# Kernel tuning notes

Hardware: AMD Instinct MI355X
Metric: run time of the kernel (lower is better)

Reference implementation:

```python
import jax, jax.numpy as jnp
import numpy as np

WS = 8        # window_size
OWIN = 12     # overlap_win_size = int(8*0.5)+8
PAD = 2       # (OWIN - WS)//2
HEADS = 4
DH = 16
INNER = HEADS * DH  # 64
DIM = 64


def _unfold(x, ws=WS, owin=OWIN, pad=PAD):
    # torch nn.Unfold(kernel=(owin,owin), stride=ws, padding=pad):
    # output [b, C*owin*owin, L] with channel ordering (c, kh, kw), L row-major over windows
    b, c, h, w = x.shape
    xp = jnp.pad(x, ((0, 0), (0, 0), (pad, pad), (pad, pad)))
    nH, nW = h // ws, w // ws
    ri = (jnp.arange(nH) * ws)[:, None] + jnp.arange(owin)[None, :]  # [nH, owin]
    ci = (jnp.arange(nW) * ws)[:, None] + jnp.arange(owin)[None, :]  # [nW, owin]
    p = xp[:, :, ri, :]          # [b, c, nH, owin, Wp]
    p = p[:, :, :, :, ci]        # [b, c, nH, owin, nW, owin]
    p = p.transpose(0, 1, 3, 5, 2, 4)  # [b, c, kh, kw, nH, nW]
    return p.reshape(b, c * owin * owin, nH * nW)


def setup_inputs() -> dict:
    key = jax.random.key(0)
    k1, k2, k3 = jax.random.split(key, 3)
    x = jax.random.normal(k1, (1, DIM, 64, 64), jnp.float32)
    w_qkv = jax.random.normal(k2, (3 * INNER, DIM), jnp.float32) * 0.05  # 1x1 conv, no bias
    w_out = jax.random.normal(k3, (DIM, INNER), jnp.float32) * 0.05     # 1x1 conv, no bias
    ln_w = jnp.ones((DIM,), jnp.float32)
    return {"x": x, "w_qkv": w_qkv, "w_out": w_out, "ln_w": ln_w}


def reference(x, w_qkv, w_out, ln_w):
    b, c, h, w = x.shape
    # BiasFree LayerNorm over channel dim (no mean subtraction)
    xc = x.transpose(0, 2, 3, 1)                       # b h w c
    var = jnp.var(xc, axis=-1, keepdims=True)
    xn = (xc / jnp.sqrt(var + 1e-5) * ln_w).transpose(0, 3, 1, 2)
    # qkv 1x1 conv
    qkv = jnp.einsum('bchw,oc->bohw', xn, w_qkv)
    qs, ks, vs = jnp.split(qkv, 3, axis=1)
    # queries: all h*w positions
    qs = qs.transpose(0, 2, 3, 1).reshape(b, h * w, HEADS, DH).transpose(0, 2, 1, 3)  # b heads N dh
    # keys/values: overlapping unfolded windows (faithful to torch reshape order)
    kk = _unfold(ks).reshape(b, INNER, -1).reshape(b, HEADS, -1, DH)  # b heads M dh
    vv = _unfold(vs).reshape(b, INNER, -1).reshape(b, HEADS, -1, DH)
    # rel_pos and fixed_mask are all-zero tensors in the source -> no-op bias
    attn = jnp.einsum('bhnd,bhmd->bhnm', qs, kk) * (DH ** -0.5)
    attn = jax.nn.softmax(attn, axis=-1)
    out = jnp.einsum('bhnm,bhmd->bhnd', attn, vv)
    out = out.transpose(0, 2, 1, 3).reshape(b, h, w, INNER).transpose(0, 3, 1, 2)
    return jnp.einsum('bchw,oc->bohw', out, w_out)
```

## Files before the change

kernel.cpp:

```cpp
#include <hip/hip_runtime.h>
#include <math.h>

#define PIX 4096
typedef unsigned short ushort_t;
typedef unsigned int uint_t;
typedef __attribute__((ext_vector_type(8))) short bf16x8;
typedef __attribute__((ext_vector_type(16))) float f32x16;

#define OFF_USHORT 2228224
#define U_QH 0
#define U_QKB 262144
#define U_KF 786432
#define U_VF 1376256

#define QSCALE 0.36067376022224087f

#if defined(__has_builtin)
#if __has_builtin(__builtin_amdgcn_exp2f)
#define EXP2F(x) __builtin_amdgcn_exp2f(x)
#endif
#if __has_builtin(__builtin_amdgcn_perm)
#define PKHI16(u1, u0) __builtin_amdgcn_perm((u1), (u0), 0x07060302u)
#endif
#endif
#ifndef EXP2F
#define EXP2F(x) exp2f(x)
#endif
#ifndef PKHI16
#define PKHI16(u1, u0) (((u0) >> 16) | ((u1) & 0xFFFF0000u))
#endif

__device__ __forceinline__ ushort_t rn_bf16(float x) {
    uint_t u = __float_as_uint(x);
    return (ushort_t)((u + 0x7FFFu + ((u >> 16) & 1u)) >> 16);
}

__global__ __launch_bounds__(256)
void k_qkv(const float* __restrict__ x, const float* __restrict__ w_qkv,
           const float* __restrict__ ln_w, ushort_t* __restrict__ QH,
           ushort_t* __restrict__ QKB)
{
    const int tid = threadIdx.x;
    const int w = tid >> 6, l = tid & 63;
    const int col = l & 31, half = l >> 5;
    const int id = (int)blockIdx.x * 4 + w;
    const int ot = id >> 7;
    const int pt = id & 127;
    const int obase = ot * 32;
    const int gpx = pt * 32 + col;

    float s = 0.f, s2 = 0.f;
    #pragma unroll 16
    for (int c = 0; c < 64; ++c) {
        float v = x[c * PIX + gpx];
        s += v; s2 = fmaf(v, v, s2);
    }
    const float mean = s * 0.015625f;
    const float var  = fmaf(-mean, mean, s2 * 0.015625f);
    const float rs   = 1.0f / sqrtf(var + 1e-5f);

    f32x16 acc = {0,0,0,0,0,0,0,0,0,0,0,0,0,0,0,0};
    const float* wrow = w_qkv + (obase + col) * 64;
    #pragma unroll
    for (int s4 = 0; s4 < 4; ++s4) {
        const int kbase = s4 * 16 + half * 8;
        float t8[8];
        *(float4*)&t8[0] = *(const float4*)&wrow[kbase];
        *(float4*)&t8[4] = *(const float4*)&wrow[kbase + 4];
        union { uint_t u[4]; bf16x8 b; } wa;
        #pragma unroll
        for (int j = 0; j < 4; ++j)
            wa.u[j] = (uint_t)rn_bf16(t8[2 * j]) | ((uint_t)rn_bf16(t8[2 * j + 1]) << 16);
        const float4 lwa = *(const float4*)&ln_w[kbase];
        const float4 lwb = *(const float4*)&ln_w[kbase + 4];
        float b8[8];
        b8[0] = x[(kbase + 0) * PIX + gpx] * rs * lwa.x;
        b8[1] = x[(kbase + 1) * PIX + gpx] * rs * lwa.y;
        b8[2] = x[(kbase + 2) * PIX + gpx] * rs * lwa.z;
        b8[3] = x[(kbase + 3) * PIX + gpx] * rs * lwa.w;
        b8[4] = x[(kbase + 4) * PIX + gpx] * rs * lwb.x;
        b8[5] = x[(kbase + 5) * PIX + gpx] * rs * lwb.y;
        b8[6] = x[(kbase + 6) * PIX + gpx] * rs * lwb.z;
        b8[7] = x[(kbase + 7) * PIX + gpx] * rs * lwb.w;
        union { uint_t u[4]; bf16x8 b; } xb;
        #pragma unroll
        for (int j = 0; j < 4; ++j)
            xb.u[j] = (uint_t)rn_bf16(b8[2 * j]) | ((uint_t)rn_bf16(b8[2 * j + 1]) << 16);
        acc = __builtin_amdgcn_mfma_f32_32x32x16_bf16(wa.b, xb.b, acc, 0, 0, 0);
    }

    #pragma unroll
    for (int j = 0; j < 16; ++j) {
        const int o = obase + (j & 3) + 8 * (j >> 2) + 4 * half;
        if (o < 64) {
            QH[((o >> 4) * PIX + gpx) * 16 + (o & 15)] = rn_bf16(acc[j] * QSCALE);
        } else {
            QKB[(o - 64) * PIX + gpx] = rn_bf16(acc[j]);
        }
    }
}

__global__ __launch_bounds__(256)
void k_prep_kv(const ushort_t* __restrict__ QKB,
               ushort_t* __restrict__ KF, ushort_t* __restrict__ VF)
{
    const int bid = blockIdx.x;
    const int tid = threadIdx.x;
    if (bid < 288) {
        const int t = bid * 256 + tid;
        const int h = t / 18432; int r = t - h * 18432;
        const int i = r >> 6;   const int l = r & 63;
        const int col = l & 31, rl = l >> 5;
        const int m = i * 32 + col;
        const int cc = m / 576;  const int r3 = m - cc * 576;
        const int orr = r3 / 48; const int r4 = r3 - orr * 48;
        const int oc = r4 >> 2, wg = r4 & 3;
        const int row = wg * 16 + rl * 8 + orr - 2;
        const bool rowOk = (unsigned)row < 64u;
        const ushort_t* src = QKB + (h * 16 + cc) * PIX + row * 64 + (oc - 2);
        union { ushort_t us[8]; bf16x8 b; } o8;
        #pragma unroll
        for (int j = 0; j < 8; ++j) {
            const int colp = j * 8 + oc - 2;
            o8.us[j] = (rowOk && (unsigned)colp < 64u) ? src[j * 8] : (ushort_t)0;
        }
        *(bf16x8*)&KF[(h * 288 + i) * 512 + l * 8] = o8.b;
    } else {
        const int t = (bid - 288) * 256 + tid;
        const int h = t / 18432; int r = t - h * 18432;
        const int i = r >> 6;   const int r2 = r & 63;
        const int half = r2 >> 5; const int rl = (r2 >> 4) & 1; const int colD = r2 & 15;
        const int d = colD;
        const int vcolp = (d & 7) * 8 - 2;
        const int rbase = (d >> 3) * 8 - 2;
        const ushort_t* srcp = QKB + (64 + h * 16) * PIX;
        union { ushort_t us[8]; bf16x8 b; } o8;
        #pragma unroll
        for (int j2 = 0; j2 < 8; ++j2) {
            const int m = i * 32 + half * 16 + rl * 4 + (j2 & 3) + 8 * (j2 >> 2);
            const int cc = m / 576;  const int r3 = m - cc * 576;
            const int orr = r3 / 48; const int r4 = r3 - orr * 48;
            const int oc = r4 >> 2, wg = r4 & 3;
            const int row  = wg * 16 + rbase + orr;
            const int colp = vcolp + oc;
            const bool ok = ((unsigned)row < 64u) && ((unsigned)colp < 64u);
            o8.us[j2] = ok ? srcp[cc * PIX + row * 64 + colp] : (ushort_t)0;
        }
        *(bf16x8*)&VF[(h * 288 + i) * 512 + half * 256 + (rl * 16 + colD) * 8] = o8.b;
    }
}

__global__ __launch_bounds__(512)
void k_attn(const ushort_t* __restrict__ QH,
            const ushort_t* __restrict__ KF, const ushort_t* __restrict__ VF,
            float* __restrict__ APart)
{
    const int tid = threadIdx.x;
    const int w   = tid >> 6;
    const int l   = tid & 63;
    const int col = l & 31;
    const int rl  = l >> 5;

    const int bid  = blockIdx.x;
    const int x    = bid & 7;
    const int h    = x >> 1;
    const int tile = ((bid >> 3) << 1) | (x & 1);
    const int qbase = tile * 64;

    const ushort_t* Qb = QH + ((h << 12) + qbase + col) * 16 + rl * 8;
    const bf16x8 qh0 = *(const bf16x8*)&Qb[0];
    const bf16x8 qh1 = *(const bf16x8*)&Qb[512];

    f32x16 acc0 = {0,0,0,0,0,0,0,0,0,0,0,0,0,0,0,0};
    f32x16 acc1 = {0,0,0,0,0,0,0,0,0,0,0,0,0,0,0,0};
    const f32x16 zero = {0,0,0,0,0,0,0,0,0,0,0,0,0,0,0,0};

    union { uint_t u[4]; bf16x8 b; } vconst;
    const uint_t cfill = (col == 16) ? 0x3F803F80u : 0u;
    vconst.u[0] = cfill; vconst.u[1] = cfill; vconst.u[2] = cfill; vconst.u[3] = cfill;

    const ushort_t* kb = KF + (h * 288 + w * 36) * 512;
    const ushort_t* vb = VF + (h * 288 + w * 36) * 512;

    bf16x8 kh = *(const bf16x8*)&kb[l * 8];
    bf16x8 v0 = vconst.b, v1 = vconst.b;
    if (col < 16) {
        v0 = *(const bf16x8*)&vb[(rl * 16 + col) * 8];
        v1 = *(const bf16x8*)&vb[256 + (rl * 16 + col) * 8];
    }

    for (int i = 0; i < 36; ++i) {
        const bf16x8 ckh = kh, cv0 = v0, cv1 = v1;
        if (i < 35) {
            kb += 512; vb += 512;
            kh = *(const bf16x8*)&kb[l * 8];
            if (col < 16) {
                v0 = *(const bf16x8*)&vb[(rl * 16 + col) * 8];
                v1 = *(const bf16x8*)&vb[256 + (rl * 16 + col) * 8];
            }
        }

        f32x16 S0 = __builtin_amdgcn_mfma_f32_32x32x16_bf16(ckh, qh0, zero, 0, 0, 0);
        f32x16 S1 = __builtin_amdgcn_mfma_f32_32x32x16_bf16(ckh, qh1, zero, 0, 0, 0);

        {
            float p[16];
            #pragma unroll
            for (int r = 0; r < 16; ++r) p[r] = EXP2F(S0[r]);
            union { uint_t u[4]; bf16x8 b; } A0, A1;
            #pragma unroll
            for (int j = 0; j < 4; ++j) {
                A0.u[j] = PKHI16(__float_as_uint(p[2 * j + 1]), __float_as_uint(p[2 * j]));
                A1.u[j] = PKHI16(__float_as_uint(p[8 + 2 * j + 1]), __float_as_uint(p[8 + 2 * j]));
            }
            acc0 = __builtin_amdgcn_mfma_f32_32x32x16_bf16(A0.b, cv0, acc0, 0, 0, 0);
            acc0 = __builtin_amdgcn_mfma_f32_32x32x16_bf16(A1.b, cv1, acc0, 0, 0, 0);
        }
        {
            float p[16];
            #pragma unroll
            for (int r = 0; r < 16; ++r) p[r] = EXP2F(S1[r]);
            union { uint_t u[4]; bf16x8 b; } A0, A1;
            #pragma unroll
            for (int j = 0; j < 4; ++j) {
                A0.u[j] = PKHI16(__float_as_uint(p[2 * j + 1]), __float_as_uint(p[2 * j]));
                A1.u[j] = PKHI16(__float_as_uint(p[8 + 2 * j + 1]), __float_as_uint(p[8 + 2 * j]));
            }
            acc1 = __builtin_amdgcn_mfma_f32_32x32x16_bf16(A0.b, cv0, acc1, 0, 0, 0);
            acc1 = __builtin_amdgcn_mfma_f32_32x32x16_bf16(A1.b, cv1, acc1, 0, 0, 0);
        }
    }

    if (col <= 16) {
        float* base = APart + ((size_t)(w * 4 + h) << 12) * 17;
        #pragma unroll
        for (int j = 0; j < 16; ++j) {
            const int q = qbase + (j & 3) + 8 * (j >> 2) + 4 * rl;
            base[q * 17 + col]        = acc0[j];
            base[(q + 32) * 17 + col] = acc1[j];
        }
    }
}

__global__ __launch_bounds__(256)
void k_proj(const float* __restrict__ APart, const float* __restrict__ w_out,
            float* __restrict__ out)
{
    __shared__ float asum[16 * 72];
    __shared__ float wo[64 * 68];
    __shared__ float as2[16 * 68];
    __shared__ float rdn[64];
    const int tid = threadIdx.x;
    const int pbase = blockIdx.x * 16;

    for (int idx = tid; idx < 1088; idx += 256) {
        int q_l = idx / 68; int rem = idx - q_l * 68;
        int h = rem / 17;  int c17 = rem - h * 17;
        float s = 0.f;
        #pragma unroll
        for (int ks = 0; ks < 8; ++ks)
            s += APart[((size_t)((ks * 4 + h) * PIX + pbase + q_l)) * 17 + c17];
        asum[q_l * 72 + h * 17 + c17] = s;
    }
    for (int idx = tid; idx < 4096; idx += 256)
        wo[(idx >> 6) * 68 + (idx & 63)] = w_out[idx];
    __syncthreads();
    if (tid < 64) {
        int h = tid >> 4, px = tid & 15;
        rdn[tid] = 1.0f / asum[px * 72 + h * 17 + 16];
    }
    __syncthreads();
    for (int idx = tid; idx < 1024; idx += 256) {
        int px = idx >> 6, ii = idx & 63;
        int h = ii >> 4, d = ii & 15;
        as2[px * 68 + ii] = asum[px * 72 + h * 17 + d] * rdn[h * 16 + px];
    }
    __syncthreads();

    const int pl = tid & 15;
    const int og = tid >> 4;
    float a0 = 0.f, a1 = 0.f, a2 = 0.f, a3 = 0.f;
    for (int c = 0; c < 64; c += 4) {
        const float4 xv = *(const float4*)&as2[pl * 68 + c];
        const float4 w0 = *(const float4*)&wo[(og * 4 + 0) * 68 + c];
        const float4 w1 = *(const float4*)&wo[(og * 4 + 1) * 68 + c];
        const float4 w2 = *(const float4*)&wo[(og * 4 + 2) * 68 + c];
        const float4 w3 = *(const float4*)&wo[(og * 4 + 3) * 68 + c];
        a0 = fmaf(xv.x, w0.x, fmaf(xv.y, w0.y, fmaf(xv.z, w0.z, fmaf(xv.w, w0.w, a0))));
        a1 = fmaf(xv.x, w1.x, fmaf(xv.y, w1.y, fmaf(xv.z, w1.z, fmaf(xv.w, w1.w, a1))));
        a2 = fmaf(xv.x, w2.x, fmaf(xv.y, w2.y, fmaf(xv.z, w2.z, fmaf(xv.w, w2.w, a2))));
        a3 = fmaf(xv.x, w3.x, fmaf(xv.y, w3.y, fmaf(xv.z, w3.z, fmaf(xv.w, w3.w, a3))));
    }
    out[(og * 4 + 0) * PIX + pbase + pl] = a0;
    out[(og * 4 + 1) * PIX + pbase + pl] = a1;
    out[(og * 4 + 2) * PIX + pbase + pl] = a2;
    out[(og * 4 + 3) * PIX + pbase + pl] = a3;
}

extern "C" void kernel_launch(void* const* d_in, const int* in_sizes, int n_in,
                              void* d_out, int out_size, void* d_ws, size_t ws_size,
                              hipStream_t stream)
{
    const float* x     = (const float*)d_in[0];
    const float* w_qkv = (const float*)d_in[1];
    const float* w_out = (const float*)d_in[2];
    const float* ln_w  = (const float*)d_in[3];
    float* out = (float*)d_out;
    float* ws  = (float*)d_ws;

    float* APart = ws;
    ushort_t* U  = (ushort_t*)(ws + OFF_USHORT);
    ushort_t* QH  = U + U_QH;
    ushort_t* QKB = U + U_QKB;
    ushort_t* KF  = U + U_KF;
    ushort_t* VF  = U + U_VF;

    k_qkv     <<<dim3(192), dim3(256), 0, stream>>>(x, w_qkv, ln_w, QH, QKB);
    k_prep_kv <<<dim3(576), dim3(256), 0, stream>>>(QKB, KF, VF);
    k_attn    <<<dim3(256), dim3(512), 0, stream>>>(QH, KF, VF, APart);
    k_proj    <<<dim3(256), dim3(256), 0, stream>>>(APart, w_out, out);
}
```

Measured before the change: 97.91 us.

## Split attention KV range across 16 waves with in-block LDS reduction

Result: faster. 91.79 us (-6.3%).

```diff
diff --git a/kernel.cpp b/kernel.cpp
--- a/kernel.cpp
+++ b/kernel.cpp
@@ -35,7 +35,7 @@
     return (ushort_t)((u + 0x7FFFu + ((u >> 16) & 1u)) >> 16);
 }
 
-__global__ __launch_bounds__(256)
+__global__ __launch_bounds__(192)
 void k_qkv(const float* __restrict__ x, const float* __restrict__ w_qkv,
            const float* __restrict__ ln_w, ushort_t* __restrict__ QH,
            ushort_t* __restrict__ QKB)
@@ -43,7 +43,7 @@
     const int tid = threadIdx.x;
     const int w = tid >> 6, l = tid & 63;
     const int col = l & 31, half = l >> 5;
-    const int id = (int)blockIdx.x * 4 + w;
+    const int id = (int)blockIdx.x * 3 + w;
     const int ot = id >> 7;
     const int pt = id & 127;
     const int obase = ot * 32;
@@ -150,11 +150,13 @@
     }
 }
 
-__global__ __launch_bounds__(512)
+__global__ __launch_bounds__(1024, 4)
 void k_attn(const ushort_t* __restrict__ QH,
             const ushort_t* __restrict__ KF, const ushort_t* __restrict__ VF,
-            float* __restrict__ APart)
-{
+            float* __restrict__ AO)
+{
+    __shared__ float racc[16][64][18];
+
     const int tid = threadIdx.x;
     const int w   = tid >> 6;
     const int l   = tid & 63;
@@ -179,24 +181,26 @@
     const uint_t cfill = (col == 16) ? 0x3F803F80u : 0u;
     vconst.u[0] = cfill; vconst.u[1] = cfill; vconst.u[2] = cfill; vconst.u[3] = cfill;
 
-    const ushort_t* kb = KF + (h * 288 + w * 36) * 512;
-    const ushort_t* vb = VF + (h * 288 + w * 36) * 512;
+    const ushort_t* kb = KF + (h * 288 + w * 18) * 512;
+    const ushort_t* vb = VF + (h * 288 + w * 18) * 512;
+    const int vl = (rl * 16 + (col & 15)) * 8;
+    const bool vload = (col < 16);
 
     bf16x8 kh = *(const bf16x8*)&kb[l * 8];
     bf16x8 v0 = vconst.b, v1 = vconst.b;
-    if (col < 16) {
-        v0 = *(const bf16x8*)&vb[(rl * 16 + col) * 8];
-        v1 = *(const bf16x8*)&vb[256 + (rl * 16 + col) * 8];
-    }
-
-    for (int i = 0; i < 36; ++i) {
+    if (vload) {
+        v0 = *(const bf16x8*)&vb[vl];
+        v1 = *(const bf16x8*)&vb[256 + vl];
+    }
+
+    for (int i = 0; i < 18; ++i) {
         const bf16x8 ckh = kh, cv0 = v0, cv1 = v1;
-        if (i < 35) {
+        if (i < 17) {
             kb += 512; vb += 512;
             kh = *(const bf16x8*)&kb[l * 8];
-            if (col < 16) {
-                v0 = *(const bf16x8*)&vb[(rl * 16 + col) * 8];
-                v1 = *(const bf16x8*)&vb[256 + (rl * 16 + col) * 8];
+            if (vload) {
+                v0 = *(const bf16x8*)&vb[vl];
+                v1 = *(const bf16x8*)&vb[256 + vl];
             }
         }
 
@@ -232,49 +236,40 @@
     }
 
     if (col <= 16) {
-        float* base = APart + ((size_t)(w * 4 + h) << 12) * 17;
         #pragma unroll
         for (int j = 0; j < 16; ++j) {
-            const int q = qbase + (j & 3) + 8 * (j >> 2) + 4 * rl;
-            base[q * 17 + col]        = acc0[j];
-            base[(q + 32) * 17 + col] = acc1[j];
-        }
-    }
+            const int q0 = (j & 3) + 8 * (j >> 2) + 4 * rl;
+            racc[w][q0][col]      = acc0[j];
+            racc[w][32 + q0][col] = acc1[j];
+        }
+    }
+    __syncthreads();
+
+    const int q = tid >> 4, d = tid & 15;
+    float sum = 0.f, den = 0.f;
+    #pragma unroll
+    for (int ww = 0; ww < 16; ++ww) {
+        sum += racc[ww][q][d];
+        den += racc[ww][q][16];
+    }
+    AO[(qbase + q) * 64 + h * 16 + d] = sum / den;
 }
 
 __global__ __launch_bounds__(256)
-void k_proj(const float* __restrict__ APart, const float* __restrict__ w_out,
+void k_proj(const float* __restrict__ AO, const float* __restrict__ w_out,
             float* __restrict__ out)
 {
-    __shared__ float asum[16 * 72];
+    __shared__ float as2[16 * 68];
     __shared__ float wo[64 * 68];
-    __shared__ float as2[16 * 68];
-    __shared__ float rdn[64];
     const int tid = threadIdx.x;
     const int pbase = blockIdx.x * 16;
 
-    for (int idx = tid; idx < 1088; idx += 256) {
-        int q_l = idx / 68; int rem = idx - q_l * 68;
-        int h = rem / 17;  int c17 = rem - h * 17;
-        float s = 0.f;
-        #pragma unroll
-        for (int ks = 0; ks < 8; ++ks)
-            s += APart[((size_t)((ks * 4 + h) * PIX + pbase + q_l)) * 17 + c17];
-        asum[q_l * 72 + h * 17 + c17] = s;
+    for (int idx = tid; idx < 1024; idx += 256) {
+        int pl = idx >> 6, i = idx & 63;
+        as2[pl * 68 + i] = AO[(pbase + pl) * 64 + i];
     }
     for (int idx = tid; idx < 4096; idx += 256)
         wo[(idx >> 6) * 68 + (idx & 63)] = w_out[idx];
-    __syncthreads();
-    if (tid < 64) {
-        int h = tid >> 4, px = tid & 15;
-        rdn[tid] = 1.0f / asum[px * 72 + h * 17 + 16];
-    }
-    __syncthreads();
-    for (int idx = tid; idx < 1024; idx += 256) {
-        int px = idx >> 6, ii = idx & 63;
-        int h = ii >> 4, d = ii & 15;
-        as2[px * 68 + ii] = asum[px * 72 + h * 17 + d] * rdn[h * 16 + px];
-    }
     __syncthreads();
 
     const int pl = tid & 15;
@@ -308,15 +303,15 @@
     float* out = (float*)d_out;
     float* ws  = (float*)d_ws;
 
-    float* APart = ws;
+    float* AO = ws;
     ushort_t* U  = (ushort_t*)(ws + OFF_USHORT);
     ushort_t* QH  = U + U_QH;
     ushort_t* QKB = U + U_QKB;
     ushort_t* KF  = U + U_KF;
     ushort_t* VF  = U + U_VF;
 
-    k_qkv     <<<dim3(192), dim3(256), 0, stream>>>(x, w_qkv, ln_w, QH, QKB);
-    k_prep_kv <<<dim3(576), dim3(256), 0, stream>>>(QKB, KF, VF);
-    k_attn    <<<dim3(256), dim3(512), 0, stream>>>(QH, KF, VF, APart);
-    k_proj    <<<dim3(256), dim3(256), 0, stream>>>(APart, w_out, out);
-}
+    k_qkv     <<<dim3(256), dim3(192),  0, stream>>>(x, w_qkv, ln_w, QH, QKB);
+    k_prep_kv <<<dim3(576), dim3(256),  0, stream>>>(QKB, KF, VF);
+    k_attn    <<<dim3(256), dim3(1024), 0, stream>>>(QH, KF, VF, AO);
+    k_proj    <<<dim3(256), dim3(256),  0, stream>>>(AO, w_out, out);
+}
```
